# Performance work log

Hardware: AMD Instinct MI355X
Metric: run time of the kernel (lower is better)

The kernel has to match this reference:

```python
import jax, jax.numpy as jnp
import numpy as np

N = 1_000_000   # pose-graph nodes
E = 2_000_000   # edges (odometry + loop closures)
M = N - 1
L1, L2, L3, L4 = 1.0, 0.1, 1.0, 0.1  # loss weights
EPS = 1e-8

# ---- quaternion / Lie-group helpers (pypose convention: [x,y,z,w]) ----

def qmul(q, r):
    qv, qw = q[..., :3], q[..., 3:]
    rv, rw = r[..., :3], r[..., 3:]
    w = qw * rw - jnp.sum(qv * rv, axis=-1, keepdims=True)
    v = qw * rv + rw * qv + jnp.cross(qv, rv)
    return jnp.concatenate([v, w], axis=-1)

def qconj(q):  # inverse of a unit quaternion
    return jnp.concatenate([-q[..., :3], q[..., 3:]], axis=-1)

def qrot(q, v):  # rotate vector v by unit quaternion q
    qv, qw = q[..., :3], q[..., 3:]
    t = 2.0 * jnp.cross(qv, v)
    return v + qw * t + jnp.cross(qv, t)

def so3_log(q):  # SO3 -> so3 rotation vector phi
    v, w = q[..., :3], q[..., 3]
    n = jnp.linalg.norm(v, axis=-1)
    theta = 2.0 * jnp.arctan2(n, w)
    big = n > EPS
    k = jnp.where(big, theta / jnp.where(big, n, 1.0), 2.0 / jnp.where(jnp.abs(w) > EPS, w, 1.0))
    return v * k[..., None]

def se3_log(t, q):  # SE3 -> se3 = [tau(3), phi(3)] (translation first, pypose order)
    phi = so3_log(q)
    theta2 = jnp.sum(phi * phi, axis=-1)
    theta = jnp.sqrt(theta2)
    small = theta < 1e-4
    ts = jnp.where(small, 1.0, theta)
    # V^{-1} coefficient: 1/theta^2 - (1+cos)/(2 theta sin); Taylor -> 1/12
    coef = jnp.where(small, 1.0 / 12.0,
                     1.0 / jnp.where(small, 1.0, theta2)
                     - (1.0 + jnp.cos(ts)) / (2.0 * ts * jnp.sin(ts)))
    pxt = jnp.cross(phi, t)
    tau = t - 0.5 * pxt + coef[..., None] * jnp.cross(phi, pxt)  # V^{-1} t without 3x3 mats
    return jnp.concatenate([tau, phi], axis=-1)

def _unit_quat(key, n):
    q = jax.random.normal(key, (n, 4), dtype=jnp.float32)
    return q / jnp.linalg.norm(q, axis=-1, keepdims=True)

def setup_inputs() -> dict:
    key = jax.random.key(0)
    k = jax.random.split(key, 9)
    nodes = jnp.concatenate([jax.random.normal(k[0], (N, 3), jnp.float32), _unit_quat(k[1], N)], axis=-1)
    vels = jax.random.normal(k[2], (N, 3), jnp.float32)
    edges = jax.random.randint(k[3], (E, 2), 0, N, dtype=jnp.int32)
    poses = jnp.concatenate([jax.random.normal(k[4], (E, 3), jnp.float32), _unit_quat(k[5], E)], axis=-1)
    imu_drots = _unit_quat(k[6], M)
    imu_dtrans = 0.1 * jax.random.normal(k[7], (M, 3), jnp.float32)
    imu_dvels = 0.1 * jax.random.normal(k[8], (M, 3), jnp.float32)
    dts = jnp.full((M, 1), 0.05, dtype=jnp.float32)
    return dict(edges=edges, nodes=nodes, vels=vels, poses=poses,
                imu_drots=imu_drots, imu_dtrans=imu_dtrans, imu_dvels=imu_dvels, dts=dts)

def reference(edges, nodes, vels, poses, imu_drots, imu_dtrans, imu_dvels, dts):
    t_n, q_n = nodes[:, :3], nodes[:, 3:]
    # --- pose-graph residual: (poses^-1 o node1^-1 o node2).Log() ---
    n1 = nodes[edges[:, 0]]
    n2 = nodes[edges[:, 1]]
    t1, q1 = n1[:, :3], n1[:, 3:]
    t2, q2 = n2[:, :3], n2[:, 3:]
    tp, qp = poses[:, :3], poses[:, 3:]
    qi1 = qconj(q1)
    ti1 = -qrot(qi1, t1)           # node1^-1
    qa = qmul(qi1, q2)
    ta = ti1 + qrot(qi1, t2)       # node1^-1 o node2
    qip = qconj(qp)
    tip = -qrot(qip, tp)           # poses^-1
    qe = qmul(qip, qa)
    te = tip + qrot(qip, ta)
    pgerr = se3_log(te, qe)                                   # [E, 6]
    # --- adjacent velocity residual ---
    adjvelerr = imu_dvels - (vels[1:] - vels[:-1])            # [M, 3]
    # --- IMU rotation residual: (drot^-1 o R1^-1 o R2).Log() ---
    qre = qmul(qconj(imu_drots), qmul(qconj(q_n[:-1]), q_n[1:]))
    imuroterr = so3_log(qre)                                  # [M, 3]
    # --- translation/velocity residual ---
    transvelerr = (t_n[1:] - t_n[:-1]) - (vels[:-1] * dts + imu_dtrans)  # [M, 3]
    return jnp.concatenate([L1 * pgerr.ravel(), L2 * adjvelerr.ravel(),
                            L3 * imuroterr.ravel(), L4 * transvelerr.ravel()], axis=0)
```

## Files before the change

kernel.cpp:

```cpp
#include <hip/hip_runtime.h>
#include <hip/hip_fp16.h>
#include <math.h>

#define EPS_Q 1e-8f

struct F3 { float x, y, z; };
struct Q4 { F3 v; float w; };

typedef float    fvec4 __attribute__((ext_vector_type(4)));
typedef unsigned uvec4 __attribute__((ext_vector_type(4)));
typedef int      ivec2 __attribute__((ext_vector_type(2)));

__device__ __forceinline__ F3 add3(F3 a, F3 b){ return {a.x+b.x, a.y+b.y, a.z+b.z}; }
__device__ __forceinline__ F3 sub3(F3 a, F3 b){ return {a.x-b.x, a.y-b.y, a.z-b.z}; }
__device__ __forceinline__ F3 scal3(float s, F3 a){ return {s*a.x, s*a.y, s*a.z}; }
__device__ __forceinline__ float dot3(F3 a, F3 b){ return a.x*b.x + a.y*b.y + a.z*b.z; }
__device__ __forceinline__ F3 cross3(F3 a, F3 b){
    return { a.y*b.z - a.z*b.y, a.z*b.x - a.x*b.z, a.x*b.y - a.y*b.x };
}

__device__ __forceinline__ Q4 qmul(Q4 q, Q4 r){
    Q4 o;
    o.w = q.w*r.w - dot3(q.v, r.v);
    o.v = add3(add3(scal3(q.w, r.v), scal3(r.w, q.v)), cross3(q.v, r.v));
    return o;
}
__device__ __forceinline__ Q4 qconj(Q4 q){ return { {-q.v.x, -q.v.y, -q.v.z}, q.w }; }
__device__ __forceinline__ F3 qrot(Q4 q, F3 v){
    F3 t = scal3(2.0f, cross3(q.v, v));
    return add3(add3(v, scal3(q.w, t)), cross3(q.v, t));
}
__device__ __forceinline__ F3 so3_log(Q4 q){
    float n = sqrtf(dot3(q.v, q.v));
    float theta = 2.0f * atan2f(n, q.w);
    float k;
    if (n > EPS_Q) k = theta / n;
    else           k = 2.0f / ((fabsf(q.w) > EPS_Q) ? q.w : 1.0f);
    return scal3(k, q.v);
}

__device__ __forceinline__ float ntl (const float* p){ return __builtin_nontemporal_load(p); }
__device__ __forceinline__ void  nts (float* p, float v){ __builtin_nontemporal_store(v, p); }

__device__ __forceinline__ unsigned pack2h(float a, float b){
    __half2 h = __floats2half2_rn(a, b);
    unsigned u; __builtin_memcpy(&u, &h, 4);
    return u;
}
__device__ __forceinline__ float2 unp2h(unsigned u){
    __half2 h; __builtin_memcpy(&h, &u, 4);
    return __half22float2(h);
}

template<bool PACK>
__global__ __launch_bounds__(256)
void prep_kernel(const float* __restrict__ nodes,
                 const float* __restrict__ vels,
                 const float* __restrict__ imu_drots,
                 const float* __restrict__ imu_dtrans,
                 const float* __restrict__ imu_dvels,
                 const float* __restrict__ dts,
                 float*       __restrict__ out,
                 uvec4*       __restrict__ nodes16,
                 int N, int M,
                 size_t off_adjvel, size_t off_imurot, size_t off_transvel)
{
    const int m = blockIdx.x * 256 + threadIdx.x;
    if (m >= N) return;

    const float* n0 = nodes + 7*(size_t)m;
    F3 t0 = {n0[0], n0[1], n0[2]};  Q4 q0 = {{n0[3], n0[4], n0[5]}, n0[6]};

    if (PACK) {
        uvec4 row = { pack2h(t0.x, t0.y), pack2h(t0.z, 0.0f),
                      pack2h(q0.v.x, q0.v.y), pack2h(q0.v.z, q0.w) };
        nodes16[m] = row;
    }

    if (m >= M) return;

    const float* n1p = nodes + 7*(size_t)(m+1);
    F3 t1 = {n1p[0], n1p[1], n1p[2]};  Q4 q1 = {{n1p[3], n1p[4], n1p[5]}, n1p[6]};

    F3 v0 = {vels[3*(size_t)m],     vels[3*(size_t)m + 1], vels[3*(size_t)m + 2]};
    F3 v1 = {vels[3*(size_t)m + 3], vels[3*(size_t)m + 4], vels[3*(size_t)m + 5]};

    fvec4 drq = __builtin_nontemporal_load(reinterpret_cast<const fvec4*>(imu_drots) + m);
    Q4 dr = {{drq.x, drq.y, drq.z}, drq.w};

    F3 dvm = { ntl(imu_dvels + 3*(size_t)m),
               ntl(imu_dvels + 3*(size_t)m + 1),
               ntl(imu_dvels + 3*(size_t)m + 2) };
    F3 dtr = { ntl(imu_dtrans + 3*(size_t)m),
               ntl(imu_dtrans + 3*(size_t)m + 1),
               ntl(imu_dtrans + 3*(size_t)m + 2) };
    float dt = ntl(dts + m);

    F3 adjv = sub3(dvm, sub3(v1, v0));
    nts(out + off_adjvel + 3*(size_t)m,     0.1f * adjv.x);
    nts(out + off_adjvel + 3*(size_t)m + 1, 0.1f * adjv.y);
    nts(out + off_adjvel + 3*(size_t)m + 2, 0.1f * adjv.z);

    Q4 qre = qmul(qconj(dr), qmul(qconj(q0), q1));
    F3 rot = so3_log(qre);
    nts(out + off_imurot + 3*(size_t)m,     rot.x);
    nts(out + off_imurot + 3*(size_t)m + 1, rot.y);
    nts(out + off_imurot + 3*(size_t)m + 2, rot.z);

    F3 tv = sub3(sub3(t1, t0), add3(scal3(dt, v0), dtr));
    nts(out + off_transvel + 3*(size_t)m,     0.1f * tv.x);
    nts(out + off_transvel + 3*(size_t)m + 1, 0.1f * tv.y);
    nts(out + off_transvel + 3*(size_t)m + 2, 0.1f * tv.z);
}

__device__ __forceinline__ void edge_math(F3 t1, Q4 q1, F3 t2, Q4 q2,
                                          F3 tp, Q4 qp, float res[6])
{
    Q4 qi1 = qconj(q1);
    F3 ti1 = scal3(-1.0f, qrot(qi1, t1));
    Q4 qa  = qmul(qi1, q2);
    F3 ta  = add3(ti1, qrot(qi1, t2));

    Q4 qip = qconj(qp);
    F3 tip = scal3(-1.0f, qrot(qip, tp));
    Q4 qe  = qmul(qip, qa);
    F3 te  = add3(tip, qrot(qip, ta));

    F3 phi = so3_log(qe);
    float theta2 = dot3(phi, phi);
    float theta  = sqrtf(theta2);
    float coef;
    if (theta < 1e-4f) {
        coef = 1.0f / 12.0f;
    } else {
        float s, c;
        sincosf(theta, &s, &c);
        coef = 1.0f / theta2 - (1.0f + c) / (2.0f * theta * s);
    }
    F3 pxt = cross3(phi, te);
    F3 tau = add3(sub3(te, scal3(0.5f, pxt)), scal3(coef, cross3(phi, pxt)));

    res[0] = tau.x; res[1] = tau.y; res[2] = tau.z;
    res[3] = phi.x; res[4] = phi.y; res[5] = phi.z;
}

__global__ __launch_bounds__(256)
void edge_kernel3(const int*   __restrict__ edges,
                  const uvec4* __restrict__ nodes16,
                  const float* __restrict__ poses,
                  float*       __restrict__ out,
                  int E)
{
    __shared__ __attribute__((aligned(16))) float sp[7*256];
    __shared__ __attribute__((aligned(16))) float so[6*256];

    const int tid   = threadIdx.x;
    const int b0    = blockIdx.x * 256;
    const int nrows = min(256, E - b0);
    const bool active = (tid < nrows);

    ivec2 ij = {0, 0};
    uvec4 r1 = {0,0,0,0}, r2 = {0,0,0,0};
    if (active) {
        ij = __builtin_nontemporal_load(reinterpret_cast<const ivec2*>(edges) + (b0 + tid));
        r1 = nodes16[ij.x];
        r2 = nodes16[ij.y];
    }

    {
        const float* src = poses + 7*(size_t)b0;
        const int ndw = nrows * 7;
        const int nx4 = ndw >> 2;
        for (int idx = tid; idx < nx4; idx += 256) {
            fvec4 v = __builtin_nontemporal_load(reinterpret_cast<const fvec4*>(src) + idx);
            reinterpret_cast<fvec4*>(sp)[idx] = v;
        }
        for (int idx = (nx4 << 2) + tid; idx < ndw; idx += 256)
            sp[idx] = ntl(src + idx);
    }
    __syncthreads();

    if (active) {
        const float* pr = sp + 7*tid;
        F3 tp = {pr[0], pr[1], pr[2]};
        Q4 qp = {{pr[3], pr[4], pr[5]}, pr[6]};

        float2 a0 = unp2h(r1.x), a1 = unp2h(r1.y), a2 = unp2h(r1.z), a3 = unp2h(r1.w);
        float2 b0f= unp2h(r2.x), b1 = unp2h(r2.y), b2 = unp2h(r2.z), b3 = unp2h(r2.w);
        F3 t1 = {a0.x, a0.y, a1.x};  Q4 q1 = {{a2.x, a2.y, a3.x}, a3.y};
        F3 t2 = {b0f.x, b0f.y, b1.x};  Q4 q2 = {{b2.x, b2.y, b3.x}, b3.y};

        float res[6];
        edge_math(t1, q1, t2, q2, tp, qp, res);
        #pragma unroll
        for (int k = 0; k < 6; ++k) so[6*tid + k] = res[k];
    }
    __syncthreads();

    {
        float* dst = out + 6*(size_t)b0;
        const int ndw = nrows * 6;
        const int nx4 = ndw >> 2;
        for (int idx = tid; idx < nx4; idx += 256) {
            fvec4 v = reinterpret_cast<const fvec4*>(so)[idx];
            __builtin_nontemporal_store(v, reinterpret_cast<fvec4*>(dst) + idx);
        }
        for (int idx = (nx4 << 2) + tid; idx < ndw; idx += 256)
            nts(dst + idx, so[idx]);
    }
}

__global__ __launch_bounds__(256)
void edge_kernel_direct(const int*   __restrict__ edges,
                        const float* __restrict__ nodes,
                        const float* __restrict__ poses,
                        float*       __restrict__ out,
                        int E)
{
    const int e = blockIdx.x * 256 + threadIdx.x;
    if (e >= E) return;

    ivec2 ij = __builtin_nontemporal_load(reinterpret_cast<const ivec2*>(edges) + e);
    const float* n1 = nodes + 7*(size_t)ij.x;
    const float* n2 = nodes + 7*(size_t)ij.y;
    const float* p  = poses + 7*(size_t)e;

    F3 t1 = {n1[0], n1[1], n1[2]};  Q4 q1 = {{n1[3], n1[4], n1[5]}, n1[6]};
    F3 t2 = {n2[0], n2[1], n2[2]};  Q4 q2 = {{n2[3], n2[4], n2[5]}, n2[6]};

    float res[6];
    edge_math(t1, q1, t2, q2,
              F3{ntl(p+0), ntl(p+1), ntl(p+2)}, Q4{{ntl(p+3), ntl(p+4), ntl(p+5)}, ntl(p+6)},
              res);
    float* o = out + 6*(size_t)e;
    #pragma unroll
    for (int k = 0; k < 6; ++k) nts(o + k, res[k]);
}

extern "C" void kernel_launch(void* const* d_in, const int* in_sizes, int n_in,
                              void* d_out, int out_size, void* d_ws, size_t ws_size,
                              hipStream_t stream) {
    const int*   edges      = (const int*)  d_in[0];
    const float* nodes      = (const float*)d_in[1];
    const float* vels       = (const float*)d_in[2];
    const float* poses      = (const float*)d_in[3];
    const float* imu_drots  = (const float*)d_in[4];
    const float* imu_dtrans = (const float*)d_in[5];
    const float* imu_dvels  = (const float*)d_in[6];
    const float* dts        = (const float*)d_in[7];
    float* out = (float*)d_out;

    const int E = in_sizes[0] / 2;
    const int N = in_sizes[1] / 7;
    const int M = in_sizes[7];

    const size_t off_adjvel   = 6*(size_t)E;
    const size_t off_imurot   = off_adjvel + 3*(size_t)M;
    const size_t off_transvel = off_imurot + 3*(size_t)M;

    const int BLK = 256;
    const int NBLKS = (N + BLK - 1) / BLK;
    const int EBLKS = (E + BLK - 1) / BLK;

    uvec4* nodes16 = (uvec4*)d_ws;
    const bool can_pack = (d_ws != nullptr) && (ws_size >= (size_t)N * 16);

    if (can_pack) {
        prep_kernel<true><<<NBLKS, BLK, 0, stream>>>(nodes, vels, imu_drots, imu_dtrans,
                                                     imu_dvels, dts, out, nodes16, N, M,
                                                     off_adjvel, off_imurot, off_transvel);
        edge_kernel3<<<EBLKS, BLK, 0, stream>>>(edges, nodes16, poses, out, E);
    } else {
        prep_kernel<false><<<NBLKS, BLK, 0, stream>>>(nodes, vels, imu_drots, imu_dtrans,
                                                      imu_dvels, dts, out, nullptr, N, M,
                                                      off_adjvel, off_imurot, off_transvel);
        edge_kernel_direct<<<EBLKS, BLK, 0, stream>>>(edges, nodes, poses, out, E);
    }
}
```

Before: 258.2 us.

## Split node packing into lean kernel and fuse IMU residuals into edge kernel

Node packing to fp16 moves into its own small kernel that stages node rows through shared memory with vector loads. The IMU and velocity residual work moves out of the prep kernel and into the edge kernel. Blocks are interleaved so node-residual blocks are spread evenly among edge blocks. The goal is a short critical path before the gather-heavy edge pass, with the streaming node work overlapping the latency-bound gathers. The cost is divergent block roles and an unchanged launch count.

```diff
diff --git a/kernel.cpp b/kernel.cpp
--- a/kernel.cpp
+++ b/kernel.cpp
@@ -52,65 +52,31 @@
     return __half22float2(h);
 }
 
-template<bool PACK>
 __global__ __launch_bounds__(256)
-void prep_kernel(const float* __restrict__ nodes,
-                 const float* __restrict__ vels,
-                 const float* __restrict__ imu_drots,
-                 const float* __restrict__ imu_dtrans,
-                 const float* __restrict__ imu_dvels,
-                 const float* __restrict__ dts,
-                 float*       __restrict__ out,
-                 uvec4*       __restrict__ nodes16,
-                 int N, int M,
-                 size_t off_adjvel, size_t off_imurot, size_t off_transvel)
-{
-    const int m = blockIdx.x * 256 + threadIdx.x;
-    if (m >= N) return;
-
-    const float* n0 = nodes + 7*(size_t)m;
-    F3 t0 = {n0[0], n0[1], n0[2]};  Q4 q0 = {{n0[3], n0[4], n0[5]}, n0[6]};
-
-    if (PACK) {
-        uvec4 row = { pack2h(t0.x, t0.y), pack2h(t0.z, 0.0f),
-                      pack2h(q0.v.x, q0.v.y), pack2h(q0.v.z, q0.w) };
-        nodes16[m] = row;
-    }
-
-    if (m >= M) return;
-
-    const float* n1p = nodes + 7*(size_t)(m+1);
-    F3 t1 = {n1p[0], n1p[1], n1p[2]};  Q4 q1 = {{n1p[3], n1p[4], n1p[5]}, n1p[6]};
-
-    F3 v0 = {vels[3*(size_t)m],     vels[3*(size_t)m + 1], vels[3*(size_t)m + 2]};
-    F3 v1 = {vels[3*(size_t)m + 3], vels[3*(size_t)m + 4], vels[3*(size_t)m + 5]};
-
-    fvec4 drq = __builtin_nontemporal_load(reinterpret_cast<const fvec4*>(imu_drots) + m);
-    Q4 dr = {{drq.x, drq.y, drq.z}, drq.w};
-
-    F3 dvm = { ntl(imu_dvels + 3*(size_t)m),
-               ntl(imu_dvels + 3*(size_t)m + 1),
-               ntl(imu_dvels + 3*(size_t)m + 2) };
-    F3 dtr = { ntl(imu_dtrans + 3*(size_t)m),
-               ntl(imu_dtrans + 3*(size_t)m + 1),
-               ntl(imu_dtrans + 3*(size_t)m + 2) };
-    float dt = ntl(dts + m);
-
-    F3 adjv = sub3(dvm, sub3(v1, v0));
-    nts(out + off_adjvel + 3*(size_t)m,     0.1f * adjv.x);
-    nts(out + off_adjvel + 3*(size_t)m + 1, 0.1f * adjv.y);
-    nts(out + off_adjvel + 3*(size_t)m + 2, 0.1f * adjv.z);
-
-    Q4 qre = qmul(qconj(dr), qmul(qconj(q0), q1));
-    F3 rot = so3_log(qre);
-    nts(out + off_imurot + 3*(size_t)m,     rot.x);
-    nts(out + off_imurot + 3*(size_t)m + 1, rot.y);
-    nts(out + off_imurot + 3*(size_t)m + 2, rot.z);
-
-    F3 tv = sub3(sub3(t1, t0), add3(scal3(dt, v0), dtr));
-    nts(out + off_transvel + 3*(size_t)m,     0.1f * tv.x);
-    nts(out + off_transvel + 3*(size_t)m + 1, 0.1f * tv.y);
-    nts(out + off_transvel + 3*(size_t)m + 2, 0.1f * tv.z);
+void pack_kernel(const float* __restrict__ nodes, uvec4* __restrict__ nodes16, int N)
+{
+    __shared__ __attribute__((aligned(16))) float s[7*256];
+    const int tid   = threadIdx.x;
+    const int base  = blockIdx.x * 256;
+    const int nrows = min(256, N - base);
+    const int ndw   = nrows * 7;
+    const int nx4   = ndw >> 2;
+
+    const float* src = nodes + 7*(size_t)base;
+    for (int idx = tid; idx < nx4; idx += 256) {
+        fvec4 v = __builtin_nontemporal_load(reinterpret_cast<const fvec4*>(src) + idx);
+        reinterpret_cast<fvec4*>(s)[idx] = v;
+    }
+    for (int idx = (nx4 << 2) + tid; idx < ndw; idx += 256)
+        s[idx] = ntl(src + idx);
+    __syncthreads();
+
+    if (tid < nrows) {
+        const float* r = s + 7*tid;
+        uvec4 row = { pack2h(r[0], r[1]), pack2h(r[2], 0.0f),
+                      pack2h(r[3], r[4]), pack2h(r[5], r[6]) };
+        nodes16[base + tid] = row;
+    }
 }
 
 __device__ __forceinline__ void edge_math(F3 t1, Q4 q1, F3 t2, Q4 q2,
@@ -145,68 +111,120 @@
 }
 
 __global__ __launch_bounds__(256)
-void edge_kernel3(const int*   __restrict__ edges,
+void fused_kernel(const int*   __restrict__ edges,
                   const uvec4* __restrict__ nodes16,
                   const float* __restrict__ poses,
+                  const float* __restrict__ nodes,
+                  const float* __restrict__ vels,
+                  const float* __restrict__ imu_drots,
+                  const float* __restrict__ imu_dtrans,
+                  const float* __restrict__ imu_dvels,
+                  const float* __restrict__ dts,
                   float*       __restrict__ out,
-                  int E)
+                  int E, int M, int NB, int T,
+                  size_t off_adjvel, size_t off_imurot, size_t off_transvel)
 {
     __shared__ __attribute__((aligned(16))) float sp[7*256];
     __shared__ __attribute__((aligned(16))) float so[6*256];
 
-    const int tid   = threadIdx.x;
-    const int b0    = blockIdx.x * 256;
-    const int nrows = min(256, E - b0);
-    const bool active = (tid < nrows);
-
-    ivec2 ij = {0, 0};
-    uvec4 r1 = {0,0,0,0}, r2 = {0,0,0,0};
-    if (active) {
-        ij = __builtin_nontemporal_load(reinterpret_cast<const ivec2*>(edges) + (b0 + tid));
-        r1 = nodes16[ij.x];
-        r2 = nodes16[ij.y];
-    }
-
-    {
-        const float* src = poses + 7*(size_t)b0;
-        const int ndw = nrows * 7;
-        const int nx4 = ndw >> 2;
-        for (int idx = tid; idx < nx4; idx += 256) {
-            fvec4 v = __builtin_nontemporal_load(reinterpret_cast<const fvec4*>(src) + idx);
-            reinterpret_cast<fvec4*>(sp)[idx] = v;
+    const int b   = blockIdx.x;
+    const int tid = threadIdx.x;
+    const long long f0 = ((long long)b       * NB) / T;
+    const long long f1 = ((long long)(b + 1) * NB) / T;
+
+    if (f1 > f0) {
+        const int m = (int)f0 * 256 + tid;
+        if (m >= M) return;
+
+        const float* n0 = nodes + 7*(size_t)m;
+        const float* n1 = nodes + 7*(size_t)(m+1);
+        F3 t0 = {n0[0], n0[1], n0[2]};  Q4 q0 = {{n0[3], n0[4], n0[5]}, n0[6]};
+        F3 t1 = {n1[0], n1[1], n1[2]};  Q4 q1 = {{n1[3], n1[4], n1[5]}, n1[6]};
+
+        F3 v0 = {vels[3*(size_t)m],     vels[3*(size_t)m + 1], vels[3*(size_t)m + 2]};
+        F3 v1 = {vels[3*(size_t)m + 3], vels[3*(size_t)m + 4], vels[3*(size_t)m + 5]};
+
+        fvec4 drq = __builtin_nontemporal_load(reinterpret_cast<const fvec4*>(imu_drots) + m);
+        Q4 dr = {{drq.x, drq.y, drq.z}, drq.w};
+
+        F3 dvm = { ntl(imu_dvels + 3*(size_t)m),
+                   ntl(imu_dvels + 3*(size_t)m + 1),
+                   ntl(imu_dvels + 3*(size_t)m + 2) };
+        F3 dtr = { ntl(imu_dtrans + 3*(size_t)m),
+                   ntl(imu_dtrans + 3*(size_t)m + 1),
+                   ntl(imu_dtrans + 3*(size_t)m + 2) };
+        float dt = ntl(dts + m);
+
+        F3 adjv = sub3(dvm, sub3(v1, v0));
+        nts(out + off_adjvel + 3*(size_t)m,     0.1f * adjv.x);
+        nts(out + off_adjvel + 3*(size_t)m + 1, 0.1f * adjv.y);
+        nts(out + off_adjvel + 3*(size_t)m + 2, 0.1f * adjv.z);
+
+        Q4 qre = qmul(qconj(dr), qmul(qconj(q0), q1));
+        F3 rot = so3_log(qre);
+        nts(out + off_imurot + 3*(size_t)m,     rot.x);
+        nts(out + off_imurot + 3*(size_t)m + 1, rot.y);
+        nts(out + off_imurot + 3*(size_t)m + 2, rot.z);
+
+        F3 tv = sub3(sub3(t1, t0), add3(scal3(dt, v0), dtr));
+        nts(out + off_transvel + 3*(size_t)m,     0.1f * tv.x);
+        nts(out + off_transvel + 3*(size_t)m + 1, 0.1f * tv.y);
+        nts(out + off_transvel + 3*(size_t)m + 2, 0.1f * tv.z);
+    } else {
+        const int eb    = b - (int)f0;
+        const int b0    = eb * 256;
+        const int nrows = min(256, E - b0);
+        const bool active = (tid < nrows);
+
+        ivec2 ij = {0, 0};
+        uvec4 r1 = {0,0,0,0}, r2 = {0,0,0,0};
+        if (active) {
+            ij = __builtin_nontemporal_load(reinterpret_cast<const ivec2*>(edges) + (b0 + tid));
+            r1 = nodes16[ij.x];
+            r2 = nodes16[ij.y];
         }
-        for (int idx = (nx4 << 2) + tid; idx < ndw; idx += 256)
-            sp[idx] = ntl(src + idx);
-    }
-    __syncthreads();
-
-    if (active) {
-        const float* pr = sp + 7*tid;
-        F3 tp = {pr[0], pr[1], pr[2]};
-        Q4 qp = {{pr[3], pr[4], pr[5]}, pr[6]};
-
-        float2 a0 = unp2h(r1.x), a1 = unp2h(r1.y), a2 = unp2h(r1.z), a3 = unp2h(r1.w);
-        float2 b0f= unp2h(r2.x), b1 = unp2h(r2.y), b2 = unp2h(r2.z), b3 = unp2h(r2.w);
-        F3 t1 = {a0.x, a0.y, a1.x};  Q4 q1 = {{a2.x, a2.y, a3.x}, a3.y};
-        F3 t2 = {b0f.x, b0f.y, b1.x};  Q4 q2 = {{b2.x, b2.y, b3.x}, b3.y};
-
-        float res[6];
-        edge_math(t1, q1, t2, q2, tp, qp, res);
-        #pragma unroll
-        for (int k = 0; k < 6; ++k) so[6*tid + k] = res[k];
-    }
-    __syncthreads();
-
-    {
-        float* dst = out + 6*(size_t)b0;
-        const int ndw = nrows * 6;
-        const int nx4 = ndw >> 2;
-        for (int idx = tid; idx < nx4; idx += 256) {
-            fvec4 v = reinterpret_cast<const fvec4*>(so)[idx];
-            __builtin_nontemporal_store(v, reinterpret_cast<fvec4*>(dst) + idx);
+
+        {
+            const float* src = poses + 7*(size_t)b0;
+            const int ndw = nrows * 7;
+            const int nx4 = ndw >> 2;
+            for (int idx = tid; idx < nx4; idx += 256) {
+                fvec4 v = __builtin_nontemporal_load(reinterpret_cast<const fvec4*>(src) + idx);
+                reinterpret_cast<fvec4*>(sp)[idx] = v;
+            }
+            for (int idx = (nx4 << 2) + tid; idx < ndw; idx += 256)
+                sp[idx] = ntl(src + idx);
         }
-        for (int idx = (nx4 << 2) + tid; idx < ndw; idx += 256)
-            nts(dst + idx, so[idx]);
+        __syncthreads();
+
+        if (active) {
+            const float* pr = sp + 7*tid;
+            F3 tp = {pr[0], pr[1], pr[2]};
+            Q4 qp = {{pr[3], pr[4], pr[5]}, pr[6]};
+
+            float2 a0 = unp2h(r1.x), a1 = unp2h(r1.y), a2 = unp2h(r1.z), a3 = unp2h(r1.w);
+            float2 c0 = unp2h(r2.x), c1 = unp2h(r2.y), c2 = unp2h(r2.z), c3 = unp2h(r2.w);
+            F3 t1 = {a0.x, a0.y, a1.x};  Q4 q1 = {{a2.x, a2.y, a3.x}, a3.y};
+            F3 t2 = {c0.x, c0.y, c1.x};  Q4 q2 = {{c2.x, c2.y, c3.x}, c3.y};
+
+            float res[6];
+            edge_math(t1, q1, t2, q2, tp, qp, res);
+            #pragma unroll
+            for (int k = 0; k < 6; ++k) so[6*tid + k] = res[k];
+        }
+        __syncthreads();
+
+        {
+            float* dst = out + 6*(size_t)b0;
+            const int ndw = nrows * 6;
+            const int nx4 = ndw >> 2;
+            for (int idx = tid; idx < nx4; idx += 256) {
+                fvec4 v = reinterpret_cast<const fvec4*>(so)[idx];
+                __builtin_nontemporal_store(v, reinterpret_cast<fvec4*>(dst) + idx);
+            }
+            for (int idx = (nx4 << 2) + tid; idx < ndw; idx += 256)
+                nts(dst + idx, so[idx]);
+        }
     }
 }
 
@@ -235,6 +253,56 @@
     float* o = out + 6*(size_t)e;
     #pragma unroll
     for (int k = 0; k < 6; ++k) nts(o + k, res[k]);
+}
+
+__global__ __launch_bounds__(256)
+void node_kernel(const float* __restrict__ nodes,
+                 const float* __restrict__ vels,
+                 const float* __restrict__ imu_drots,
+                 const float* __restrict__ imu_dtrans,
+                 const float* __restrict__ imu_dvels,
+                 const float* __restrict__ dts,
+                 float*       __restrict__ out,
+                 int M,
+                 size_t off_adjvel, size_t off_imurot, size_t off_transvel)
+{
+    const int m = blockIdx.x * 256 + threadIdx.x;
+    if (m >= M) return;
+
+    const float* n0 = nodes + 7*(size_t)m;
+    const float* n1 = nodes + 7*(size_t)(m+1);
+    F3 t0 = {n0[0], n0[1], n0[2]};  Q4 q0 = {{n0[3], n0[4], n0[5]}, n0[6]};
+    F3 t1 = {n1[0], n1[1], n1[2]};  Q4 q1 = {{n1[3], n1[4], n1[5]}, n1[6]};
+
+    F3 v0 = {vels[3*(size_t)m],     vels[3*(size_t)m + 1], vels[3*(size_t)m + 2]};
+    F3 v1 = {vels[3*(size_t)m + 3], vels[3*(size_t)m + 4], vels[3*(size_t)m + 5]};
+
+    fvec4 drq = __builtin_nontemporal_load(reinterpret_cast<const fvec4*>(imu_drots) + m);
+    Q4 dr = {{drq.x, drq.y, drq.z}, drq.w};
+
+    F3 dvm = { ntl(imu_dvels + 3*(size_t)m),
+               ntl(imu_dvels + 3*(size_t)m + 1),
+               ntl(imu_dvels + 3*(size_t)m + 2) };
+    F3 dtr = { ntl(imu_dtrans + 3*(size_t)m),
+               ntl(imu_dtrans + 3*(size_t)m + 1),
+               ntl(imu_dtrans + 3*(size_t)m + 2) };
+    float dt = ntl(dts + m);
+
+    F3 adjv = sub3(dvm, sub3(v1, v0));
+    nts(out + off_adjvel + 3*(size_t)m,     0.1f * adjv.x);
+    nts(out + off_adjvel + 3*(size_t)m + 1, 0.1f * adjv.y);
+    nts(out + off_adjvel + 3*(size_t)m + 2, 0.1f * adjv.z);
+
+    Q4 qre = qmul(qconj(dr), qmul(qconj(q0), q1));
+    F3 rot = so3_log(qre);
+    nts(out + off_imurot + 3*(size_t)m,     rot.x);
+    nts(out + off_imurot + 3*(size_t)m + 1, rot.y);
+    nts(out + off_imurot + 3*(size_t)m + 2, rot.z);
+
+    F3 tv = sub3(sub3(t1, t0), add3(scal3(dt, v0), dtr));
+    nts(out + off_transvel + 3*(size_t)m,     0.1f * tv.x);
+    nts(out + off_transvel + 3*(size_t)m + 1, 0.1f * tv.y);
+    nts(out + off_transvel + 3*(size_t)m + 2, 0.1f * tv.z);
 }
 
 extern "C" void kernel_launch(void* const* d_in, const int* in_sizes, int n_in,
@@ -259,21 +327,23 @@
     const size_t off_transvel = off_imurot + 3*(size_t)M;
 
     const int BLK = 256;
-    const int NBLKS = (N + BLK - 1) / BLK;
-    const int EBLKS = (E + BLK - 1) / BLK;
+    const int EB = (E + BLK - 1) / BLK;
+    const int NB = (M + BLK - 1) / BLK;
+    const int T  = EB + NB;
 
     uvec4* nodes16 = (uvec4*)d_ws;
     const bool can_pack = (d_ws != nullptr) && (ws_size >= (size_t)N * 16);
 
     if (can_pack) {
-        prep_kernel<true><<<NBLKS, BLK, 0, stream>>>(nodes, vels, imu_drots, imu_dtrans,
-                                                     imu_dvels, dts, out, nodes16, N, M,
-                                                     off_adjvel, off_imurot, off_transvel);
-        edge_kernel3<<<EBLKS, BLK, 0, stream>>>(edges, nodes16, poses, out, E);
+        pack_kernel<<<(N + BLK - 1)/BLK, BLK, 0, stream>>>(nodes, nodes16, N);
+        fused_kernel<<<T, BLK, 0, stream>>>(edges, nodes16, poses,
+                                            nodes, vels, imu_drots, imu_dtrans,
+                                            imu_dvels, dts, out, E, M, NB, T,
+                                            off_adjvel, off_imurot, off_transvel);
     } else {
-        prep_kernel<false><<<NBLKS, BLK, 0, stream>>>(nodes, vels, imu_drots, imu_dtrans,
-                                                      imu_dvels, dts, out, nullptr, N, M,
-                                                      off_adjvel, off_imurot, off_transvel);
-        edge_kernel_direct<<<EBLKS, BLK, 0, stream>>>(edges, nodes, poses, out, E);
-    }
-}
+        edge_kernel_direct<<<EB, BLK, 0, stream>>>(edges, nodes, poses, out, E);
+        node_kernel<<<NB, BLK, 0, stream>>>(nodes, vels, imu_drots, imu_dtrans,
+                                            imu_dvels, dts, out, M,
+                                            off_adjvel, off_imurot, off_transvel);
+    }
+}
```

Result: no change. 258.2 us (+0.0%).
